# Performance work log

Hardware: AMD Instinct MI355X
Metric: run time of the kernel (lower is better)

## Reference

```python
import jax, jax.numpy as jnp
import numpy as np

B, S, D, H, FF, V, L = 2, 2048, 1024, 16, 4096, 32000, 4
HD = D // H
SCALE = HD ** -0.5
STD = 0.02


def _ln(x, w, b, eps=1e-5):
    mu = jnp.mean(x, axis=-1, keepdims=True)
    var = jnp.mean(jnp.square(x - mu), axis=-1, keepdims=True)
    return (x - mu) * jax.lax.rsqrt(var + eps) * w + b


def setup_inputs() -> dict:
    key = jax.random.key(0)
    ks = iter(jax.random.split(key, 16))

    def w(k, shape):
        return jax.random.normal(k, shape, jnp.float32) * STD

    inp = {
        "tokens": jax.random.randint(next(ks), (B, S), 0, V, jnp.int32),
        "tok_emb": w(next(ks), (V, D)),
        "ln_e_w": jnp.ones((D,), jnp.float32),
        "ln_e_b": jnp.zeros((D,), jnp.float32),
        "ln1_w": jnp.ones((L, D), jnp.float32),
        "ln1_b": jnp.zeros((L, D), jnp.float32),
        "wq": w(next(ks), (L, D, D)),
        "bq": jnp.zeros((L, D), jnp.float32),
        "wk": w(next(ks), (L, D, D)),
        "bk": jnp.zeros((L, D), jnp.float32),
        "wv": w(next(ks), (L, D, D)),
        "bv": jnp.zeros((L, D), jnp.float32),
        "wo": w(next(ks), (L, D, D)),
        "bo": jnp.zeros((L, D), jnp.float32),
        "ln2_w": jnp.ones((L, D), jnp.float32),
        "ln2_b": jnp.zeros((L, D), jnp.float32),
        "w1": w(next(ks), (L, D, 2 * FF)),
        "b1": jnp.zeros((L, 2 * FF), jnp.float32),
        "w2": w(next(ks), (L, FF, D)),
        "b2": jnp.zeros((L, D), jnp.float32),
        "lnf_w": jnp.ones((D,), jnp.float32),
        "lnf_b": jnp.zeros((D,), jnp.float32),
        "w_out": w(next(ks), (D, V)),
        "b_out": jnp.zeros((V,), jnp.float32),
    }
    return inp


def reference(tokens, tok_emb, ln_e_w, ln_e_b, ln1_w, ln1_b, wq, bq, wk, bk,
              wv, bv, wo, bo, ln2_w, ln2_b, w1, b1, w2, b2, lnf_w, lnf_b,
              w_out, b_out):
    x = tok_emb[tokens]                      # [B,S,D]
    x = _ln(x, ln_e_w, ln_e_b)               # embedding LayerNorm (dropout off)
    for l in range(L):
        # pre-LN attention
        h = _ln(x, ln1_w[l], ln1_b[l])
        q = (h @ wq[l] + bq[l]).reshape(B, S, H, HD)
        k = (h @ wk[l] + bk[l]).reshape(B, S, H, HD)
        v = (h @ wv[l] + bv[l]).reshape(B, S, H, HD)
        scores = jnp.einsum('bqhd,bkhd->bhqk', q, k) * SCALE
        attn = jax.nn.softmax(scores, axis=-1)
        o = jnp.einsum('bhqk,bkhd->bqhd', attn, v).reshape(B, S, D)
        x = x + (o @ wo[l] + bo[l])
        # pre-LN gated (GeGLU) FFN
        h = _ln(x, ln2_w[l], ln2_b[l])
        gv = h @ w1[l] + b1[l]               # [B,S,2*FF]
        gate, val = gv[..., :FF], gv[..., FF:]
        ff = jax.nn.gelu(gate, approximate=False) * val
        x = x + (ff @ w2[l] + b2[l])
    x = _ln(x, lnf_w, lnf_b)
    return x @ w_out + b_out                 # logits [B,S,V]
```

## Files before the change

kernel.cpp:

```cpp
#include <hip/hip_runtime.h>

typedef __attribute__((ext_vector_type(8))) short s16x8;
typedef __attribute__((ext_vector_type(4))) short s16x4;
typedef __attribute__((ext_vector_type(4))) float f32x4;

__device__ __forceinline__ unsigned short f2bf(float f){
    union{float f;unsigned u;}v; v.f=f;
    unsigned u=v.u;
    unsigned r=(u+0x7fffu+((u>>16)&1u))>>16;
    return (unsigned short)r;
}
__device__ __forceinline__ float bf2f(unsigned short s){
    union{unsigned u;float f;}v; v.u=((unsigned)s)<<16; return v.f;
}
__device__ __forceinline__ unsigned pk2t(float a, float b){
    return (__float_as_uint(a)>>16) | (__float_as_uint(b) & 0xffff0000u);
}
__device__ __forceinline__ unsigned pk2r(float a, float b){
    return (unsigned)f2bf(a) | ((unsigned)f2bf(b)<<16);
}
__device__ __forceinline__ f32x4 fmax4(f32x4 a, f32x4 b){
    f32x4 r; r[0]=fmaxf(a[0],b[0]); r[1]=fmaxf(a[1],b[1]);
    r[2]=fmaxf(a[2],b[2]); r[3]=fmaxf(a[3],b[3]); return r;
}

__device__ __forceinline__ void gl16(const void* g, void* l){
    __builtin_amdgcn_global_load_lds(
        (const __attribute__((address_space(1))) void*)g,
        (__attribute__((address_space(3))) void*)l, 16, 0, 0);
}

#define ATT_SCALE 0.125f

__global__ __launch_bounds__(256) void flash_k(
    const unsigned short* __restrict__ qkv,
    const unsigned short* __restrict__ vt,
    unsigned short* __restrict__ o)
{
    __shared__ __align__(16) unsigned short Pl[4][2048];
    const int t=threadIdx.x, w=t>>6, lane=t&63;
    const int lr=lane&15, lg=lane>>4;
    const int zb=blockIdx.y>>4, zh=blockIdx.y&15;
    const long sr0 = (long)zb*2048 + blockIdx.x*128 + w*32;
    const unsigned short* qb    = qkv + sr0*3072 + zh*64;
    const unsigned short* kbase = qkv + ((long)zb*2048)*3072 + 1024 + zh*64;
    const unsigned short* vtb   = vt + (long)zb*2097152 + (long)zh*131072;

    s16x8 qf[2][2];
    #pragma unroll
    for(int qg=0;qg<2;qg++)
        #pragma unroll
        for(int kc=0;kc<2;kc++)
            qf[qg][kc] = *(const s16x8*)(qb + (qg*16+lr)*3072 + kc*32 + lg*8);

    float m0=-1e30f, m1=-1e30f, l0=0.f, l1=0.f;
    f32x4 oa[2][4];
    #pragma unroll
    for(int qg=0;qg<2;qg++)
        #pragma unroll
        for(int dt=0;dt<4;dt++) oa[qg][dt]=f32x4{0.f,0.f,0.f,0.f};

    char* Pw = (char*)&Pl[w][0];
    const int swz = (lr&7)<<4;

    for(int kv0=0; kv0<2048; kv0+=64){
        f32x4 s[2][4];
        __builtin_amdgcn_s_setprio(1);
        #pragma unroll
        for(int kb=0;kb<4;kb++){
            const unsigned short* kr = kbase + (long)(kv0+kb*16+lr)*3072;
            s16x8 a0 = *(const s16x8*)(kr + lg*8);
            s16x8 a1 = *(const s16x8*)(kr + 32 + lg*8);
            #pragma unroll
            for(int qg=0;qg<2;qg++){
                f32x4 z4{0.f,0.f,0.f,0.f};
                z4 = __builtin_amdgcn_mfma_f32_16x16x32_bf16(a0, qf[qg][0], z4,0,0,0);
                s[qg][kb] = __builtin_amdgcn_mfma_f32_16x16x32_bf16(a1, qf[qg][1], z4,0,0,0);
            }
        }
        __builtin_amdgcn_s_setprio(0);
        s16x8 vreg[4][2];
        #pragma unroll
        for(int dt=0;dt<4;dt++){
            const unsigned short* vr = vtb + (dt*16+lr)*2048 + kv0;
            vreg[dt][0] = *(const s16x8*)(vr + lg*8);
            vreg[dt][1] = *(const s16x8*)(vr + 32 + lg*8);
        }
        #pragma unroll
        for(int qg=0;qg<2;qg++){
            float& m = qg? m1:m0;
            float& l = qg? l1:l0;
            f32x4 mx4 = fmax4(fmax4(s[qg][0],s[qg][1]),fmax4(s[qg][2],s[qg][3]));
            float bm = fmaxf(fmaxf(mx4[0],mx4[1]),fmaxf(mx4[2],mx4[3]));
            bm = fmaxf(bm, __shfl_xor(bm,16));
            bm = fmaxf(bm, __shfl_xor(bm,32));
            const float mn = fmaxf(m, bm);
            const float sc = __expf((m-mn)*ATT_SCALE);
            m = mn;
            float rs=0.f;
            #pragma unroll
            for(int kb=0;kb<4;kb++){
                f32x4 p;
                #pragma unroll
                for(int r=0;r<4;r++){ p[r]=__expf((s[qg][kb][r]-mn)*ATT_SCALE); rs+=p[r]; }
                s[qg][kb]=p;
            }
            rs += __shfl_xor(rs,16);
            rs += __shfl_xor(rs,32);
            l = l*sc + rs;
            #pragma unroll
            for(int dt=0;dt<4;dt++) oa[qg][dt] = oa[qg][dt]*sc;
            #pragma unroll
            for(int kb=0;kb<4;kb++){
                uint2 pw;
                pw.x = pk2t(s[qg][kb][0], s[qg][kb][1]);
                pw.y = pk2t(s[qg][kb][2], s[qg][kb][3]);
                *(uint2*)(Pw + (qg*16+lr)*128 + ((kb*32+lg*8)^swz)) = pw;
            }
        }
        asm volatile("s_waitcnt lgkmcnt(0)" ::: "memory");
        s16x8 pb0[2], pb1[2];
        #pragma unroll
        for(int qg=0;qg<2;qg++){
            pb0[qg] = *(const s16x8*)(Pw + (qg*16+lr)*128 + ((     lg*16)^swz));
            pb1[qg] = *(const s16x8*)(Pw + (qg*16+lr)*128 + ((64 + lg*16)^swz));
        }
        __builtin_amdgcn_s_setprio(1);
        #pragma unroll
        for(int dt=0;dt<4;dt++){
            #pragma unroll
            for(int qg=0;qg<2;qg++){
                oa[qg][dt] = __builtin_amdgcn_mfma_f32_16x16x32_bf16(vreg[dt][0], pb0[qg], oa[qg][dt],0,0,0);
                oa[qg][dt] = __builtin_amdgcn_mfma_f32_16x16x32_bf16(vreg[dt][1], pb1[qg], oa[qg][dt],0,0,0);
            }
        }
        __builtin_amdgcn_s_setprio(0);
    }
    #pragma unroll
    for(int qg=0;qg<2;qg++){
        const float inv = 1.f/(qg? l1:l0);
        #pragma unroll
        for(int dt=0;dt<4;dt++){
            uint2 st;
            st.x = pk2r(oa[qg][dt][0]*inv, oa[qg][dt][1]*inv);
            st.y = pk2r(oa[qg][dt][2]*inv, oa[qg][dt][3]*inv);
            *(uint2*)(o + (sr0+qg*16+lr)*1024 + zh*64 + dt*16 + lg*4) = st;
        }
    }
}

template<bool OBF16,bool BIAS,bool GEGLU>
__global__ __launch_bounds__(512,2) void gemm8_k(
    const unsigned short* __restrict__ A,
    const unsigned short* __restrict__ B,
    const float* __restrict__ bias,
    void* __restrict__ Cp,
    int K,int lda,int ldb,int ldc)
{
    __shared__ __align__(16) char lds[131072];
    const int t=threadIdx.x, w=t>>6, lane=t&63;
    const int wr=w>>2, wc=w&3;
    const int lr=lane&15, lg=lane>>4;

    const int nwg = gridDim.x*gridDim.y;
    const int id  = blockIdx.y*gridDim.x + blockIdx.x;
    const int nid = (id&7)*(nwg>>3) + (id>>3);
    const long row0 = (long)(nid % gridDim.x)*256;
    const long col0 = (long)(nid / gridDim.x)*256;

    const int NT = K>>6;

    const int csw0 = (lg*16) ^ ((lr&7)<<4);
    const int aRow = (wr*64+lr)*128;
    const int bRow = (wc*32+lr)*128;

    const int sro = t>>3;
    const int sce = (((t&7) ^ ((t>>3)&7))<<3);

#define STAGE(gp, ld_, lb) do{ \
    const unsigned short* _g=(gp); char* _l=(lb); \
    gl16(_g + (long)sro*(ld_) + sce, _l + t*16); \
    gl16(_g + (long)(sro+64)*(ld_) + sce, _l + 8192 + t*16); }while(0)

#define LDA8(m,kk) (*(const s16x8*)(Ab_ + aRow + ((m)&3)*2048 + ((m)>>2)*16384 + ((kk)? (csw0^64):csw0)))
#define LDB8(n,kk) (*(const s16x8*)(Bb_ + bRow + ((n)&1)*2048 + ((n)>>1)*16384 + ((kk)? (csw0^64):csw0)))

    f32x4 acc[8][4];
    #pragma unroll
    for(int m=0;m<8;m++)
        #pragma unroll
        for(int n=0;n<4;n++) acc[m][n]=f32x4{0.f,0.f,0.f,0.f};

    STAGE(A + row0*lda,        lda, lds);
    STAGE(B + col0*ldb,        ldb, lds+65536);
    STAGE(A + (row0+128)*lda,  lda, lds+16384);
    STAGE(B + (col0+128)*ldb,  ldb, lds+65536+16384);
    STAGE(A + row0*lda + 64,   lda, lds+32768);
    STAGE(B + col0*ldb + 64,   ldb, lds+65536+32768);
    asm volatile("s_waitcnt vmcnt(4)" ::: "memory");
    __builtin_amdgcn_s_barrier();

    for(int tt=0; tt<NT; ++tt){
        char* Ab_ = lds + ((tt&1)<<15);
        char* Bb_ = lds + 65536 + ((tt&1)<<15);
        char* An  = lds + (((tt+1)&1)<<15);
        char* Bn  = lds + 65536 + (((tt+1)&1)<<15);
        const int k1=(tt+1)<<6, k2=(tt+2)<<6;
        s16x8 a[4][2], b[4][2];

        #pragma unroll
        for(int m=0;m<4;m++){ a[m][0]=LDA8(m,0); a[m][1]=LDA8(m,1); }
        #pragma unroll
        for(int n=0;n<4;n++){ b[n][0]=LDB8(n,0); b[n][1]=LDB8(n,1); }
        if(tt+1<NT){
            STAGE(A + (row0+128)*lda + k1, lda, An+16384);
            STAGE(B + (col0+128)*ldb + k1, ldb, Bn+16384);
        }
        __builtin_amdgcn_s_barrier();
        __builtin_amdgcn_s_setprio(1);
        #pragma unroll
        for(int kk=0;kk<2;kk++)
            #pragma unroll
            for(int m=0;m<4;m++)
                #pragma unroll
                for(int n=0;n<4;n++)
                    acc[m][n]=__builtin_amdgcn_mfma_f32_16x16x32_bf16(a[m][kk],b[n][kk],acc[m][n],0,0,0);
        __builtin_amdgcn_s_setprio(0);
        __builtin_amdgcn_s_barrier();

        #pragma unroll
        for(int m=0;m<4;m++){ a[m][0]=LDA8(m+4,0); a[m][1]=LDA8(m+4,1); }
        if(tt+2<NT){
            STAGE(A + row0*lda + k2, lda, Ab_);
            STAGE(B + col0*ldb + k2, ldb, Bb_);
        }
        __builtin_amdgcn_s_barrier();
        __builtin_amdgcn_s_setprio(1);
        #pragma unroll
        for(int kk=0;kk<2;kk++)
            #pragma unroll
            for(int m=0;m<4;m++)
                #pragma unroll
                for(int n=0;n<4;n++)
                    acc[m+4][n]=__builtin_amdgcn_mfma_f32_16x16x32_bf16(a[m][kk],b[n][kk],acc[m+4][n],0,0,0);
        __builtin_amdgcn_s_setprio(0);
        if(tt+2<NT) asm volatile("s_waitcnt vmcnt(4)" ::: "memory");
        else        asm volatile("s_waitcnt vmcnt(0)" ::: "memory");
        __builtin_amdgcn_s_barrier();
    }

    if constexpr(GEGLU){
        const long hc0 = col0>>1;
        #pragma unroll
        for(int m=0;m<8;m++){
            #pragma unroll
            for(int n=0;n<2;n++){
                #pragma unroll
                for(int rr=0;rr<4;rr++){
                    const long grow = row0 + wr*64 + (m&3)*16 + (m>>2)*128 + lg*4 + rr;
                    const long g    = hc0 + wc*32 + n*16 + lr;
                    float gg = acc[m][n][rr]   + bias[g];
                    float vl = acc[m][n+2][rr] + bias[4096+g];
                    float ge = 0.5f*gg*(1.f+erff(gg*0.70710678118654752f));
                    ((unsigned short*)Cp)[grow*(long)ldc + g] = f2bf(ge*vl);
                }
            }
        }
    } else if constexpr(!OBF16){
        float* L = (float*)lds;
        const int lc4 = (t&63)<<2;
        f32x4 bv{0.f,0.f,0.f,0.f};
        if constexpr(BIAS) bv = *(const f32x4*)(bias + col0 + lc4);
        #pragma unroll
        for(int ch=0; ch<2; ch++){
            __builtin_amdgcn_s_barrier();
            #pragma unroll
            for(int mm=0;mm<4;mm++){
                #pragma unroll
                for(int n=0;n<4;n++){
                    #pragma unroll
                    for(int rr=0;rr<4;rr++){
                        const int lrow = wr*64 + mm*16 + lg*4 + rr;
                        const int lcol = wc*32 + (n&1)*16 + (n>>1)*128 + lr;
                        const int pc = ((((lcol>>2) ^ (lrow&7))<<2) | (lcol&3));
                        L[lrow*256 + pc] = acc[ch*4+mm][n][rr];
                    }
                }
            }
            __builtin_amdgcn_s_barrier();
            #pragma unroll
            for(int p=0;p<16;p++){
                const int lrow = p*8 + (t>>6);
                const int pc4 = (((lc4>>2) ^ (lrow&7))<<2);
                f32x4 v4 = *(const f32x4*)(L + lrow*256 + pc4);
                if constexpr(BIAS){ v4[0]+=bv[0]; v4[1]+=bv[1]; v4[2]+=bv[2]; v4[3]+=bv[3]; }
                __builtin_nontemporal_store(v4,
                    (f32x4*)((float*)Cp + (row0 + ch*128 + lrow)*(long)ldc + col0 + lc4));
            }
        }
    } else {
        #pragma unroll
        for(int m=0;m<8;m++){
            #pragma unroll
            for(int n=0;n<4;n++){
                #pragma unroll
                for(int rr=0;rr<4;rr++){
                    const long grow = row0 + wr*64 + (m&3)*16 + (m>>2)*128 + lg*4 + rr;
                    const long gcol = col0 + wc*32 + (n&1)*16 + (n>>1)*128 + lr;
                    float vv = acc[m][n][rr];
                    if constexpr(BIAS) vv += bias[gcol];
                    ((unsigned short*)Cp)[grow*(long)ldc+gcol]=f2bf(vv);
                }
            }
        }
    }
#undef STAGE
#undef LDA8
#undef LDB8
}

__global__ __launch_bounds__(256) void cat3_k(const float* __restrict__ a,
    const float* __restrict__ b, const float* __restrict__ c,
    float* __restrict__ out)
{
    const int i = blockIdx.x*256+threadIdx.x;
    const int l = i/3072, cc = i%3072;
    float v = (cc<1024)? a[l*1024+cc] : (cc<2048)? b[l*1024+cc-1024] : c[l*1024+cc-2048];
    out[i]=v;
}

template<int BM,int BN,int WN,bool BIAS,bool RES,bool OBF16,bool SCL,bool SWAP,bool GEGLU>
__global__ __launch_bounds__(256) void gemm_bt(
    const unsigned short* __restrict__ A,
    const unsigned short* __restrict__ B,
    const unsigned short* __restrict__ B2,
    const float* __restrict__ bias,
    const float* __restrict__ res,
    void* __restrict__ Cp,
    int K,int lda,int ldb,int ldc,
    long aSb,long aSh,long bSb,long bSh,long cSb,long cSh,int zH)
{
    constexpr int BK=64;
    constexpr int WM=4/WN, WTM=BM/WM, WTN=BN/WN;
    constexpr int FM=WTM/16, FN=WTN/16;
    constexpr int CA=BM/8, CB=BN/8;
    __shared__ __align__(16) unsigned short As[BM*BK];
    __shared__ __align__(16) unsigned short Bs[BN*BK*(GEGLU?2:1)];

    const int t=threadIdx.x, w=t>>6, lane=t&63;
    const int wr=w/WN, wc=w%WN;
    const int lr=lane&15, lg=lane>>4;
    const int z=blockIdx.z, zb=z/zH, zh=z%zH;
    const long row0 = SWAP ? (long)blockIdx.x*BM : (long)blockIdx.y*BM;
    const long col0 = SWAP ? (long)blockIdx.y*BN : (long)blockIdx.x*BN;

    const unsigned short* Ab = A + zb*aSb + zh*aSh;
    const unsigned short* Bb = B + zb*bSb + zh*bSh;

    const int lr8 = lane>>3;
    const int lc8 = (lane&7)<<3;

    f32x4 acc[FM][FN];
    f32x4 acc2[GEGLU?FM:1][GEGLU?FN:1];
    #pragma unroll
    for(int i=0;i<FM;i++)
        #pragma unroll
        for(int j=0;j<FN;j++){
            acc[i][j]=f32x4{0.f,0.f,0.f,0.f};
            if constexpr(GEGLU) acc2[i][j]=f32x4{0.f,0.f,0.f,0.f};
        }

    const int NT=K/BK;
    for(int kt=0;kt<NT;kt++){
        const int kb=kt*BK;
        #pragma unroll
        for(int cc=0;cc<CA/4;cc++){
            const int c=cc*4+w;
            gl16(Ab + (row0 + c*8 + lr8)*(long)lda + kb + lc8, (char*)As + c*1024);
        }
        #pragma unroll
        for(int cc=0;cc<CB/4;cc++){
            const int c=cc*4+w;
            gl16(Bb + (col0 + c*8 + lr8)*(long)ldb + kb + lc8, (char*)Bs + c*1024);
        }
        if constexpr(GEGLU){
            #pragma unroll
            for(int cc=0;cc<CB/4;cc++){
                const int c=cc*4+w;
                gl16(B2 + (col0 + c*8 + lr8)*(long)ldb + kb + lc8,
                     (char*)Bs + (CB + c)*1024);
            }
        }
        __syncthreads();
        const unsigned short* Arp = As + (wr*WTM+lr)*BK + lg*8;
        const unsigned short* Brp = Bs + (wc*WTN+lr)*BK + lg*8;
        #pragma unroll
        for(int kk=0;kk<2;kk++){
            s16x8 af[FM], bfv[FN], bf2[GEGLU?FN:1];
            #pragma unroll
            for(int i=0;i<FM;i++) af[i] = *(const s16x8*)(Arp + i*16*BK + kk*32);
            #pragma unroll
            for(int j=0;j<FN;j++) bfv[j]= *(const s16x8*)(Brp + j*16*BK + kk*32);
            if constexpr(GEGLU){
                #pragma unroll
                for(int j=0;j<FN;j++) bf2[j]=*(const s16x8*)(Brp + BN*BK + j*16*BK + kk*32);
            }
            #pragma unroll
            for(int i=0;i<FM;i++)
                #pragma unroll
                for(int j=0;j<FN;j++){
                    acc[i][j]=__builtin_amdgcn_mfma_f32_16x16x32_bf16(af[i],bfv[j],acc[i][j],0,0,0);
                    if constexpr(GEGLU)
                        acc2[i][j]=__builtin_amdgcn_mfma_f32_16x16x32_bf16(af[i],bf2[j],acc2[i][j],0,0,0);
                }
        }
        __syncthreads();
    }
    #pragma unroll
    for(int i=0;i<FM;i++){
        #pragma unroll
        for(int j=0;j<FN;j++){
            #pragma unroll
            for(int r=0;r<4;r++){
                const long grow = row0 + wr*WTM + i*16 + lg*4 + r;
                const long gcol = col0 + wc*WTN + j*16 + lr;
                if constexpr(GEGLU){
                    float g  = acc[i][j][r]  + bias[gcol];
                    float vl = acc2[i][j][r] + bias[gcol+4096];
                    float ge = 0.5f*g*(1.f+erff(g*0.70710678118654752f));
                    ((unsigned short*)Cp)[grow*ldc+gcol] = f2bf(ge*vl);
                } else {
                    float vv=acc[i][j][r];
                    if constexpr(SCL)  vv*=ATT_SCALE;
                    if constexpr(BIAS) vv+=bias[gcol];
                    if constexpr(RES)  vv+=res[grow*ldc+gcol];
                    const long cidx = zb*cSb + zh*cSh + grow*ldc + gcol;
                    if constexpr(OBF16) ((unsigned short*)Cp)[cidx]=f2bf(vv);
                    else                ((float*)Cp)[cidx]=vv;
                }
            }
        }
    }
}

template<bool IN32, bool REMAP>
__global__ __launch_bounds__(256) void tr_k(const void* __restrict__ in,
    unsigned short* __restrict__ out, int ldin, int ldout,
    long inZb, long inZh, long outZb, long outZh, int zH)
{
    __shared__ unsigned short tl[64][66];
    const int t=threadIdx.x;
    const int z=blockIdx.z, zb=z/zH, zh=z%zH;
    const long ib=(long)blockIdx.x*64*ldin + (long)blockIdx.y*64 + zb*inZb + zh*inZh;
    long orow = (long)blockIdx.y*64;
    if constexpr(REMAP){
        orow = (orow < 4096) ? ((orow>>7)*256 + (orow&127))
                             : (((orow-4096)>>7)*256 + 128 + ((orow-4096)&127));
    }
    const long ob=orow*ldout + (long)blockIdx.x*64 + zb*outZb + zh*outZh;
    const int r0=t>>3, c8=(t&7)*8;
    #pragma unroll
    for(int p=0;p<2;p++){
        const int rr=r0+p*32;
        if constexpr(IN32){
            f32x4 v0=*(const f32x4*)((const float*)in + ib + (long)rr*ldin + c8);
            f32x4 v1=*(const f32x4*)((const float*)in + ib + (long)rr*ldin + c8+4);
            #pragma unroll
            for(int i=0;i<4;i++){ tl[c8+i][rr]=f2bf(v0[i]); tl[c8+4+i][rr]=f2bf(v1[i]); }
        } else {
            s16x8 v=*(const s16x8*)((const unsigned short*)in + ib + (long)rr*ldin + c8);
            #pragma unroll
            for(int i=0;i<8;i++) tl[c8+i][rr]=(unsigned short)v[i];
        }
    }
    __syncthreads();
    #pragma unroll
    for(int p=0;p<2;p++){
        const int rr=r0+p*32;
        s16x8 o8;
        #pragma unroll
        for(int i=0;i<8;i++) o8[i]=(short)tl[rr][c8+i];
        *(s16x8*)(out + ob + (long)rr*ldout + c8)=o8;
    }
}

template<bool GATHER, bool OBF16>
__global__ __launch_bounds__(256) void ln_k(const float* __restrict__ in,
    const float* __restrict__ w, const float* __restrict__ b,
    void* __restrict__ out, const int* __restrict__ tok)
{
    const int row = blockIdx.x, t = threadIdx.x;
    const float* src;
    if constexpr (GATHER) src = in + (long)tok[row]*1024;
    else                  src = in + (long)row*1024;
    const int c = t*4;
    f32x4 xv = *(const f32x4*)(src + c);
    float s  = xv[0]+xv[1]+xv[2]+xv[3];
    float qq = xv[0]*xv[0]+xv[1]*xv[1]+xv[2]*xv[2]+xv[3]*xv[3];
    #pragma unroll
    for(int m=32;m;m>>=1){ s += __shfl_xor(s,m); qq += __shfl_xor(qq,m); }
    __shared__ float rs_[4], rq_[4];
    if((t&63)==0){ rs_[t>>6]=s; rq_[t>>6]=qq; }
    __syncthreads();
    s  = rs_[0]+rs_[1]+rs_[2]+rs_[3];
    qq = rq_[0]+rq_[1]+rq_[2]+rq_[3];
    const float mu = s*(1.f/1024.f);
    const float rstd = rsqrtf(qq*(1.f/1024.f)-mu*mu + 1e-5f);
    f32x4 wv = *(const f32x4*)(w+c), bv = *(const f32x4*)(b+c);
    if constexpr (OBF16){
        s16x4 ov;
        #pragma unroll
        for(int i=0;i<4;i++) ov[i]=(short)f2bf((xv[i]-mu)*rstd*wv[i]+bv[i]);
        *(s16x4*)((unsigned short*)out + (long)row*1024 + c) = ov;
    } else {
        f32x4 ov;
        #pragma unroll
        for(int i=0;i<4;i++) ov[i]=(xv[i]-mu)*rstd*wv[i]+bv[i];
        *(f32x4*)((float*)out + (long)row*1024 + c) = ov;
    }
}

template<int BM,int BN,int WN,bool BIAS>
__global__ __launch_bounds__(256) void gemm_k(
    const unsigned short* __restrict__ A,
    const float* __restrict__ Bp,
    const float* __restrict__ bias,
    float* __restrict__ Cp,
    int K,int lda,int ldb,int ldc)
{
    constexpr int BK=64, PAD=24, LDS_=BK+PAD;
    constexpr int WM = 4/WN;
    constexpr int WTM = BM/WM, WTN = BN/WN;
    constexpr int FM = WTM/16, FN = WTN/16;
    __shared__ unsigned short As[BM*LDS_];
    __shared__ unsigned short Bs[BN*LDS_];

    const int t = threadIdx.x;
    const int w = t>>6, lane = t&63;
    const int wr = w / WN, wc = w % WN;
    const int lr = lane & 15, lg = lane >> 4;

    const long row0 = (long)blockIdx.y*BM;
    const long col0 = (long)blockIdx.x*BN;

    f32x4 acc[FM][FN];
    #pragma unroll
    for(int i=0;i<FM;i++)
        #pragma unroll
        for(int j=0;j<FN;j++) acc[i][j] = f32x4{0.f,0.f,0.f,0.f};

    const int NT = K/BK;
    for(int kt=0; kt<NT; ++kt){
        const int kb = kt*BK;
        {
            constexpr int PASS = BM*BK/(256*4);
            #pragma unroll
            for(int p=0;p<PASS;p++){
                int idx = (p*256+t)*4;
                int r = idx/BK, c = idx%BK;
                *(s16x4*)&As[r*LDS_+c] = *(const s16x4*)(A + (row0+r)*lda + kb + c);
            }
        }
        {
            constexpr int TPB = 256/BN;
            constexpr int KC  = BK/TPB;
            const int n = t % BN, k0 = (t/BN)*KC;
            #pragma unroll
            for(int j0=0;j0<KC;j0+=8){
                s16x8 pk;
                #pragma unroll
                for(int i=0;i<8;i++){
                    const long gk = (long)kb + k0 + j0 + i;
                    pk[i] = (short)f2bf(Bp[gk*ldb + col0 + n]);
                }
                *(s16x8*)&Bs[n*LDS_ + k0 + j0] = pk;
            }
        }
        __syncthreads();
        const unsigned short* Ar = &As[(wr*WTM + lr)*LDS_ + lg*8];
        const unsigned short* Br = &Bs[(wc*WTN + lr)*LDS_ + lg*8];
        #pragma unroll
        for(int kk=0;kk<BK/32;kk++){
            s16x8 af[FM], bfv[FN];
            #pragma unroll
            for(int i=0;i<FM;i++) af[i]  = *(const s16x8*)(Ar + i*16*LDS_ + kk*32);
            #pragma unroll
            for(int j=0;j<FN;j++) bfv[j] = *(const s16x8*)(Br + j*16*LDS_ + kk*32);
            #pragma unroll
            for(int i=0;i<FM;i++)
                #pragma unroll
                for(int j=0;j<FN;j++)
                    acc[i][j] = __builtin_amdgcn_mfma_f32_16x16x32_bf16(af[i],bfv[j],acc[i][j],0,0,0);
        }
        __syncthreads();
    }
    #pragma unroll
    for(int i=0;i<FM;i++){
        #pragma unroll
        for(int j=0;j<FN;j++){
            #pragma unroll
            for(int r=0;r<4;r++){
                long grow = row0 + wr*WTM + i*16 + lg*4 + r;
                long gcol = col0 + wc*WTN + j*16 + lr;
                float vv = acc[i][j][r];
                if constexpr (BIAS) vv += bias[gcol];
                Cp[grow*ldc + gcol] = vv;
            }
        }
    }
}

extern "C" void kernel_launch(void* const* d_in, const int* in_sizes, int n_in,
                              void* d_out, int out_size, void* d_ws, size_t ws_size,
                              hipStream_t stream)
{
    const int*   tokens  = (const int*)  d_in[0];
    const float* tok_emb = (const float*)d_in[1];
    const float* ln_e_w  = (const float*)d_in[2];
    const float* ln_e_b  = (const float*)d_in[3];
    const float* ln1_w   = (const float*)d_in[4];
    const float* ln1_b   = (const float*)d_in[5];
    const float* wq      = (const float*)d_in[6];
    const float* bq      = (const float*)d_in[7];
    const float* wk      = (const float*)d_in[8];
    const float* bk      = (const float*)d_in[9];
    const float* wv      = (const float*)d_in[10];
    const float* bv      = (const float*)d_in[11];
    const float* wo      = (const float*)d_in[12];
    const float* bo      = (const float*)d_in[13];
    const float* ln2_w   = (const float*)d_in[14];
    const float* ln2_b   = (const float*)d_in[15];
    const float* w1      = (const float*)d_in[16];
    const float* b1      = (const float*)d_in[17];
    const float* w2      = (const float*)d_in[18];
    const float* b2      = (const float*)d_in[19];
    const float* lnf_w   = (const float*)d_in[20];
    const float* lnf_b   = (const float*)d_in[21];
    const float* w_out   = (const float*)d_in[22];
    const float* b_out   = (const float*)d_in[23];

    const int D=1024;
    const long DD  = (long)D*D;
    const long WQKV_L = 3145728L;

    unsigned short *wqkvT,*woT,*w1T,*w2T,*woutT=nullptr;
    float *x,*bqkv;
    unsigned short *h,*qkv,*vt,*o,*ff;
    bool fastTier;
    if (ws_size >= 301989888ull){
        char* p=(char*)d_ws;
        wqkvT=(unsigned short*)(p);
        woT  =(unsigned short*)(p+25165824);
        w1T  =(unsigned short*)(p+33554432);
        w2T  =(unsigned short*)(p+100663296);
        woutT=(unsigned short*)(p+134217728);
        x    =(float*)(p+201326592);
        h    =(unsigned short*)(p+218103808);
        qkv  =(unsigned short*)(p+226492416);
        vt   =(unsigned short*)(p+251658240);
        o    =(unsigned short*)(p+260046848);
        ff   =(unsigned short*)(p+268435456);
        bqkv =(float*)((char*)d_out + 134217728);
        fastTier=true;
    } else {
        char* p=(char*)d_out;
        qkv  =(unsigned short*)(p);
        bqkv =(float*)(p+25165824);
        wqkvT=(unsigned short*)(p+268435456);
        woT  =(unsigned short*)(p+293601280);
        w1T  =(unsigned short*)(p+301989888);
        w2T  =(unsigned short*)(p+369098752);
        x    =(float*)(p+402653184);
        vt   =(unsigned short*)(p+444596224);
        o    =(unsigned short*)(p+452984832);
        ff   =(unsigned short*)(p+461373440);
        h    =(unsigned short*)d_ws;
        fastTier=false;
    }

    const dim3 blk(256,1,1), blk8(512,1,1);

    tr_k<true,false><<<dim3(16,16,4), blk,0,stream>>>(wq, wqkvT,         1024,1024, DD,0, WQKV_L,0, 1);
    tr_k<true,false><<<dim3(16,16,4), blk,0,stream>>>(wk, wqkvT+1048576, 1024,1024, DD,0, WQKV_L,0, 1);
    tr_k<true,false><<<dim3(16,16,4), blk,0,stream>>>(wv, wqkvT+2097152, 1024,1024, DD,0, WQKV_L,0, 1);
    tr_k<true,false><<<dim3(16,16,4), blk,0,stream>>>(wo, woT, 1024,1024, DD,0, DD,0, 1);
    if (fastTier){
        tr_k<true,true><<<dim3(16,128,4),blk,0,stream>>>(w1, w1T, 8192,1024, 8388608L,0, 8388608L,0, 1);
        tr_k<true,false><<<dim3(16,500,1),blk,0,stream>>>(w_out, woutT, 32000,1024, 0,0, 0,0, 1);
    } else {
        tr_k<true,false><<<dim3(16,128,4),blk,0,stream>>>(w1, w1T, 8192,1024, 8388608L,0, 8388608L,0, 1);
    }
    tr_k<true,false><<<dim3(64,16,4), blk,0,stream>>>(w2, w2T, 1024,4096, 4194304L,0, 4194304L,0, 1);
    cat3_k<<<48,blk,0,stream>>>(bq, bk, bv, bqkv);

    ln_k<true,false><<<4096,blk,0,stream>>>(tok_emb, ln_e_w, ln_e_b, x, tokens);

    const dim3 g_d(8,32,1);

    for(int l=0;l<4;l++){
        ln_k<false,true><<<4096,blk,0,stream>>>(x, ln1_w+l*D, ln1_b+l*D, h, nullptr);
        gemm8_k<true,true,false><<<dim3(16,12,1),blk8,0,stream>>>(
            h, wqkvT+l*WQKV_L, bqkv+l*3072, qkv, 1024, 1024,1024,3072);
        tr_k<false,false><<<dim3(32,1,32),blk,0,stream>>>(qkv+2048, vt, 3072,2048,
            2048L*3072,64, 2097152L,131072L, 16);
        flash_k<<<dim3(16,32,1),blk,0,stream>>>(qkv, vt, o);
        gemm_bt<128,128,2,true,true,false,false,false,false><<<g_d,blk,0,stream>>>(
            o, woT+l*DD, nullptr, bo+l*D, x, x, 1024, 1024,1024,1024, 0,0,0,0,0,0, 1);
        ln_k<false,true><<<4096,blk,0,stream>>>(x, ln2_w+l*D, ln2_b+l*D, h, nullptr);
        if (fastTier){
            gemm8_k<true,true,true><<<dim3(16,32,1),blk8,0,stream>>>(
                h, w1T+l*8388608L, b1+(long)l*8192, ff, 1024, 1024,1024,4096);
        } else {
            gemm_bt<128,64,1,true,false,true,false,false,true><<<dim3(64,32,1),blk,0,stream>>>(
                h, w1T+l*8388608L, w1T+l*8388608L+4194304L, b1+(long)l*8192, nullptr, ff,
                1024, 1024,1024,4096, 0,0,0,0,0,0, 1);
        }
        gemm_bt<128,128,2,true,true,false,false,false,false><<<g_d,blk,0,stream>>>(
            ff, w2T+l*4194304L, nullptr, b2+l*D, x, x, 4096, 4096,4096,1024, 0,0,0,0,0,0, 1);
    }

    ln_k<false,true><<<4096,blk,0,stream>>>(x, lnf_w, lnf_b, h, nullptr);

    if (fastTier){
        gemm8_k<false,true,false><<<dim3(16,125,1),blk8,0,stream>>>(
            h, woutT, b_out, (float*)d_out, 1024, 1024,1024,32000);
    } else {
        gemm_k<128,128,2,true><<<dim3(250,32,1),blk,0,stream>>>(
            h, w_out, b_out, (float*)d_out, 1024, 1024,32000,32000);
    }
}
```

Before: 1.956 ms.

## Use persistent column-looping kernel for output projection; switch QKV GEMM to gemm_bt

Adds gemm8p_k, a persistent variant of the 256x256 bf16 GEMM launched with 256 blocks. Each block owns a 256-row strip and loops over 7-8 column tiles, which removes the wave-quantization tail of the previous 16x125 grid for the 32000-wide logits projection. The QKV projection moves from gemm8_k (192 blocks) to the 128x128 gemm_bt with a 24x32 grid for better CU coverage. The LDS-staged fp32 epilogue is removed from gemm8_k, so any fp32 output path there now uses plain scalar stores.

```diff
diff --git a/kernel.cpp b/kernel.cpp
--- a/kernel.cpp
+++ b/kernel.cpp
@@ -266,38 +266,6 @@
                 }
             }
         }
-    } else if constexpr(!OBF16){
-        float* L = (float*)lds;
-        const int lc4 = (t&63)<<2;
-        f32x4 bv{0.f,0.f,0.f,0.f};
-        if constexpr(BIAS) bv = *(const f32x4*)(bias + col0 + lc4);
-        #pragma unroll
-        for(int ch=0; ch<2; ch++){
-            __builtin_amdgcn_s_barrier();
-            #pragma unroll
-            for(int mm=0;mm<4;mm++){
-                #pragma unroll
-                for(int n=0;n<4;n++){
-                    #pragma unroll
-                    for(int rr=0;rr<4;rr++){
-                        const int lrow = wr*64 + mm*16 + lg*4 + rr;
-                        const int lcol = wc*32 + (n&1)*16 + (n>>1)*128 + lr;
-                        const int pc = ((((lcol>>2) ^ (lrow&7))<<2) | (lcol&3));
-                        L[lrow*256 + pc] = acc[ch*4+mm][n][rr];
-                    }
-                }
-            }
-            __builtin_amdgcn_s_barrier();
-            #pragma unroll
-            for(int p=0;p<16;p++){
-                const int lrow = p*8 + (t>>6);
-                const int pc4 = (((lc4>>2) ^ (lrow&7))<<2);
-                f32x4 v4 = *(const f32x4*)(L + lrow*256 + pc4);
-                if constexpr(BIAS){ v4[0]+=bv[0]; v4[1]+=bv[1]; v4[2]+=bv[2]; v4[3]+=bv[3]; }
-                __builtin_nontemporal_store(v4,
-                    (f32x4*)((float*)Cp + (row0 + ch*128 + lrow)*(long)ldc + col0 + lc4));
-            }
-        }
     } else {
         #pragma unroll
         for(int m=0;m<8;m++){
@@ -309,9 +277,150 @@
                     const long gcol = col0 + wc*32 + (n&1)*16 + (n>>1)*128 + lr;
                     float vv = acc[m][n][rr];
                     if constexpr(BIAS) vv += bias[gcol];
-                    ((unsigned short*)Cp)[grow*(long)ldc+gcol]=f2bf(vv);
+                    if constexpr(OBF16) ((unsigned short*)Cp)[grow*(long)ldc+gcol]=f2bf(vv);
+                    else                ((float*)Cp)[grow*(long)ldc+gcol]=vv;
                 }
             }
+        }
+    }
+#undef STAGE
+#undef LDA8
+#undef LDB8
+}
+
+__global__ __launch_bounds__(512,2) void gemm8p_k(
+    const unsigned short* __restrict__ A,
+    const unsigned short* __restrict__ B,
+    const float* __restrict__ bias,
+    float* __restrict__ Cp,
+    int K,int lda,int ldb,int ldc)
+{
+    __shared__ __align__(16) char lds[131072];
+    const int t=threadIdx.x, w=t>>6, lane=t&63;
+    const int wr=w>>2, wc=w&3;
+    const int lr=lane&15, lg=lane>>4;
+
+    const int id  = blockIdx.x;
+    const int nid = (id&7)*32 + (id>>3);
+    const long row0 = (long)(nid & 15)*256;
+    const int cg = nid>>4;
+    const int ncols = (cg<13)? 8 : 7;
+    const int c0 = cg*8 - ((cg>13)? (cg-13) : 0);
+
+    const int NT = K>>6;
+    const int csw0 = (lg*16) ^ ((lr&7)<<4);
+    const int aRow = (wr*64+lr)*128;
+    const int bRow = (wc*32+lr)*128;
+    const int sro = t>>3;
+    const int sce = (((t&7) ^ ((t>>3)&7))<<3);
+    const int lc4 = (t&63)<<2;
+
+#define STAGE(gp, ld_, lb) do{ \
+    const unsigned short* _g=(gp); char* _l=(lb); \
+    gl16(_g + (long)sro*(ld_) + sce, _l + t*16); \
+    gl16(_g + (long)(sro+64)*(ld_) + sce, _l + 8192 + t*16); }while(0)
+
+#define LDA8(m,kk) (*(const s16x8*)(Ab_ + aRow + ((m)&3)*2048 + ((m)>>2)*16384 + ((kk)? (csw0^64):csw0)))
+#define LDB8(n,kk) (*(const s16x8*)(Bb_ + bRow + ((n)&1)*2048 + ((n)>>1)*16384 + ((kk)? (csw0^64):csw0)))
+
+    for(int ci=0; ci<ncols; ci++){
+        const long col0 = (long)(c0+ci)*256;
+
+        f32x4 acc[8][4];
+        #pragma unroll
+        for(int m=0;m<8;m++)
+            #pragma unroll
+            for(int n=0;n<4;n++) acc[m][n]=f32x4{0.f,0.f,0.f,0.f};
+
+        STAGE(A + row0*lda,        lda, lds);
+        STAGE(B + col0*ldb,        ldb, lds+65536);
+        STAGE(A + (row0+128)*lda,  lda, lds+16384);
+        STAGE(B + (col0+128)*ldb,  ldb, lds+65536+16384);
+        STAGE(A + row0*lda + 64,   lda, lds+32768);
+        STAGE(B + col0*ldb + 64,   ldb, lds+65536+32768);
+        asm volatile("s_waitcnt vmcnt(4)" ::: "memory");
+        __builtin_amdgcn_s_barrier();
+
+        for(int tt=0; tt<NT; ++tt){
+            char* Ab_ = lds + ((tt&1)<<15);
+            char* Bb_ = lds + 65536 + ((tt&1)<<15);
+            char* An  = lds + (((tt+1)&1)<<15);
+            char* Bn  = lds + 65536 + (((tt+1)&1)<<15);
+            const int k1=(tt+1)<<6, k2=(tt+2)<<6;
+            s16x8 a[4][2], b[4][2];
+
+            #pragma unroll
+            for(int m=0;m<4;m++){ a[m][0]=LDA8(m,0); a[m][1]=LDA8(m,1); }
+            #pragma unroll
+            for(int n=0;n<4;n++){ b[n][0]=LDB8(n,0); b[n][1]=LDB8(n,1); }
+            if(tt+1<NT){
+                STAGE(A + (row0+128)*lda + k1, lda, An+16384);
+                STAGE(B + (col0+128)*ldb + k1, ldb, Bn+16384);
+            }
+            __builtin_amdgcn_s_barrier();
+            __builtin_amdgcn_s_setprio(1);
+            #pragma unroll
+            for(int kk=0;kk<2;kk++)
+                #pragma unroll
+                for(int m=0;m<4;m++)
+                    #pragma unroll
+                    for(int n=0;n<4;n++)
+                        acc[m][n]=__builtin_amdgcn_mfma_f32_16x16x32_bf16(a[m][kk],b[n][kk],acc[m][n],0,0,0);
+            __builtin_amdgcn_s_setprio(0);
+            __builtin_amdgcn_s_barrier();
+
+            #pragma unroll
+            for(int m=0;m<4;m++){ a[m][0]=LDA8(m+4,0); a[m][1]=LDA8(m+4,1); }
+            if(tt+2<NT){
+                STAGE(A + row0*lda + k2, lda, Ab_);
+                STAGE(B + col0*ldb + k2, ldb, Bb_);
+            }
+            __builtin_amdgcn_s_barrier();
+            __builtin_amdgcn_s_setprio(1);
+            #pragma unroll
+            for(int kk=0;kk<2;kk++)
+                #pragma unroll
+                for(int m=0;m<4;m++)
+                    #pragma unroll
+                    for(int n=0;n<4;n++)
+                        acc[m+4][n]=__builtin_amdgcn_mfma_f32_16x16x32_bf16(a[m][kk],b[n][kk],acc[m+4][n],0,0,0);
+            __builtin_amdgcn_s_setprio(0);
+            if(tt+2<NT) asm volatile("s_waitcnt vmcnt(4)" ::: "memory");
+            else        asm volatile("s_waitcnt vmcnt(0)" ::: "memory");
+            __builtin_amdgcn_s_barrier();
+        }
+
+        {
+            float* L = (float*)lds;
+            f32x4 bv = *(const f32x4*)(bias + col0 + lc4);
+            #pragma unroll
+            for(int ch=0; ch<2; ch++){
+                __builtin_amdgcn_s_barrier();
+                #pragma unroll
+                for(int mm=0;mm<4;mm++){
+                    #pragma unroll
+                    for(int n=0;n<4;n++){
+                        #pragma unroll
+                        for(int rr=0;rr<4;rr++){
+                            const int lrow = wr*64 + mm*16 + lg*4 + rr;
+                            const int lcol = wc*32 + (n&1)*16 + (n>>1)*128 + lr;
+                            const int pc = ((((lcol>>2) ^ (lrow&7))<<2) | (lcol&3));
+                            L[lrow*256 + pc] = acc[ch*4+mm][n][rr];
+                        }
+                    }
+                }
+                __builtin_amdgcn_s_barrier();
+                #pragma unroll
+                for(int p=0;p<16;p++){
+                    const int lrow = p*8 + (t>>6);
+                    const int pc4 = (((lc4>>2) ^ (lrow&7))<<2);
+                    f32x4 v4 = *(const f32x4*)(L + lrow*256 + pc4);
+                    v4[0]+=bv[0]; v4[1]+=bv[1]; v4[2]+=bv[2]; v4[3]+=bv[3];
+                    __builtin_nontemporal_store(v4,
+                        (f32x4*)(Cp + (row0 + ch*128 + lrow)*(long)ldc + col0 + lc4));
+                }
+            }
+            __builtin_amdgcn_s_barrier();
         }
     }
 #undef STAGE
@@ -699,8 +808,9 @@
 
     for(int l=0;l<4;l++){
         ln_k<false,true><<<4096,blk,0,stream>>>(x, ln1_w+l*D, ln1_b+l*D, h, nullptr);
-        gemm8_k<true,true,false><<<dim3(16,12,1),blk8,0,stream>>>(
-            h, wqkvT+l*WQKV_L, bqkv+l*3072, qkv, 1024, 1024,1024,3072);
+        gemm_bt<128,128,2,true,false,true,false,false,false><<<dim3(24,32,1),blk,0,stream>>>(
+            h, wqkvT+l*WQKV_L, nullptr, bqkv+l*3072, nullptr, qkv,
+            1024, 1024,1024,3072, 0,0,0,0,0,0, 1);
         tr_k<false,false><<<dim3(32,1,32),blk,0,stream>>>(qkv+2048, vt, 3072,2048,
             2048L*3072,64, 2097152L,131072L, 16);
         flash_k<<<dim3(16,32,1),blk,0,stream>>>(qkv, vt, o);
@@ -722,7 +832,7 @@
     ln_k<false,true><<<4096,blk,0,stream>>>(x, lnf_w, lnf_b, h, nullptr);
 
     if (fastTier){
-        gemm8_k<false,true,false><<<dim3(16,125,1),blk8,0,stream>>>(
+        gemm8p_k<<<dim3(256,1,1),blk8,0,stream>>>(
             h, woutT, b_out, (float*)d_out, 1024, 1024,1024,32000);
     } else {
         gemm_k<128,128,2,true><<<dim3(250,32,1),blk,0,stream>>>(
```

Result: slower. 2.169 ms (+10.9%).
